# Kernel optimization log

Hardware: AMD Instinct MI355X
Metric: run time of the kernel (lower is better)

Reference implementation:

```python
import jax, jax.numpy as jnp
import numpy as np

V, E, H, L, B, T = 8192, 64, 256, 2, 4, 512


def setup_inputs() -> dict:
    key = jax.random.key(0)
    ks = jax.random.split(key, 20)
    s = 0.02
    emb = (jax.random.normal(ks[0], (V, E)) * s).at[0].set(0.0)  # padding_idx=0
    x = jax.random.randint(ks[1], (B, T), 0, V)
    return {
        "x": x,
        "emb": emb,
        "W_ih0": jax.random.normal(ks[2], (H, E)) * s,
        "W_hh0": jax.random.normal(ks[3], (H, H)) * s,
        "b_ih0": jnp.zeros((H,), jnp.float32),
        "b_hh0": jnp.zeros((H,), jnp.float32),
        "W_ih1": jax.random.normal(ks[4], (H, H)) * s,
        "W_hh1": jax.random.normal(ks[5], (H, H)) * s,
        "b_ih1": jnp.zeros((H,), jnp.float32),
        "b_hh1": jnp.zeros((H,), jnp.float32),
        "Wq": jax.random.normal(ks[6], (H, H)) * s,
        "Wk": jax.random.normal(ks[7], (H, H)) * s,
        "v": jax.random.normal(ks[8], (H,)) * s,
        "gamma": jnp.ones((2 * H,), jnp.float32),
        "beta": jnp.zeros((2 * H,), jnp.float32),
        "Wfc": jax.random.normal(ks[9], (V, 2 * H)) * s,
        "bfc": jnp.zeros((V,), jnp.float32),
    }


def _rnn_layer(xs, W_ih, W_hh, b_ih, b_hh):
    # xs: (B, T, D) -> ys: (B, T, H), hT: (B, H). Vanilla tanh RNN.
    Bn = xs.shape[0]
    Hn = W_hh.shape[0]
    h0 = jnp.zeros((Bn, Hn), xs.dtype)

    def step(h, xt):
        h_new = jnp.tanh(xt @ W_ih.T + b_ih + h @ W_hh.T + b_hh)
        return h_new, h_new

    hT, ys = jax.lax.scan(step, h0, jnp.swapaxes(xs, 0, 1))
    return jnp.swapaxes(ys, 0, 1), hT


def reference(x, emb, W_ih0, W_hh0, b_ih0, b_hh0, W_ih1, W_hh1, b_ih1, b_hh1,
              Wq, Wk, v, gamma, beta, Wfc, bfc):
    # Dropout layers are identity (eval mode).
    e = emb[x]                                   # (B, T, E)
    y0, h0 = _rnn_layer(e, W_ih0, W_hh0, b_ih0, b_hh0)
    y1, h1 = _rnn_layer(y0, W_ih1, W_hh1, b_ih1, b_hh1)  # (B, T, H)

    # Bahdanau additive attention with causal mask
    q = y1 @ Wq.T                                # (B, T, H)
    k = y1 @ Wk.T                                # (B, T, H)
    # (B, Tq, Tk, H) broadcast add -> tanh -> contract with v
    scores = jnp.einsum('bijh,h->bij', jnp.tanh(q[:, :, None, :] + k[:, None, :, :]), v)
    Tn = scores.shape[1]
    causal = jnp.tril(jnp.ones((Tn, Tn), bool))
    scores = jnp.where(causal[None], scores, jnp.float32(-1e9))
    alpha = jax.nn.softmax(scores, axis=-1)      # (B, Tq, Tk)
    ctx = jnp.einsum('bij,bjh->bih', alpha, y1)  # bmm(alpha, K) with K = rnn_out

    cat = jnp.concatenate([y1, ctx], axis=-1)    # (B, T, 2H)
    mu = cat.mean(-1, keepdims=True)
    var = ((cat - mu) ** 2).mean(-1, keepdims=True)
    normed = (cat - mu) / jnp.sqrt(var + 1e-5) * gamma + beta

    logits = normed @ Wfc.T + bfc                # (B, T, V)
    h = jnp.stack([h0, h1], axis=0)              # (L, B, H)
    return logits, h
```

## Files before the change

### kernel.cpp

```cpp
#include <hip/hip_runtime.h>
#include <hip/hip_bf16.h>

typedef __bf16 bf16x8 __attribute__((ext_vector_type(8)));
typedef float  f32x4  __attribute__((ext_vector_type(4)));
typedef unsigned short u16;

#define T_N 512
#define H_N 256
#define B_N 4
#define V_N 8192
#define E_N 64

__device__ __forceinline__ float tanh_fast(float x) {
    float e = __expf(2.0f * x);
    return 1.0f - __fdividef(2.0f, e + 1.0f);
}

__device__ __forceinline__ float tanh_pade(float x) {
    x = fminf(3.0f, fmaxf(-3.0f, x));
    float x2 = x * x;
    float num = x * (945.0f + x2 * (105.0f + x2));
    float den = 945.0f + x2 * (420.0f + 15.0f * x2);
    return num * __frcp_rn(den);
}

__device__ __forceinline__ u16 f2bf(float f) {
    __hip_bfloat16 h = __float2bfloat16(f);
    return __builtin_bit_cast(u16, h);
}

__device__ __forceinline__ bf16x8 as_bf16x8(uint4 u) {
    return __builtin_bit_cast(bf16x8, u);
}

__device__ __forceinline__ uint4 pack_bf8(f32x4 lo, f32x4 hi) {
    union { u16 s[8]; uint4 u; } r;
    #pragma unroll
    for (int e = 0; e < 4; ++e) { r.s[e] = f2bf(lo[e]); r.s[e+4] = f2bf(hi[e]); }
    return r.u;
}

__device__ __forceinline__ f32x4 mfma16(bf16x8 a, bf16x8 b, f32x4 c) {
    return __builtin_amdgcn_mfma_f32_16x16x32_bf16(a, b, c, 0, 0, 0);
}

__global__ void cvt_bf16_kernel(const float* __restrict__ src, u16* __restrict__ dst, int n4) {
    int i = blockIdx.x * 256 + threadIdx.x;
    if (i < n4) {
        f32x4 v = ((const f32x4*)src)[i];
        union { u16 s[4]; unsigned long long u; } r;
        #pragma unroll
        for (int e = 0; e < 4; ++e) r.s[e] = f2bf(v[e]);
        ((unsigned long long*)dst)[i] = r.u;
    }
}

__global__ __launch_bounds__(256)
void prep_wih1_kernel(const float* __restrict__ Wih1, uint4* __restrict__ out) {
    const int f = blockIdx.x * 256 + threadIdx.x;
    const int jt = f >> 9, kk = (f >> 6) & 7, lo = f & 63;
    const int mo = lo & 15, go = lo >> 4;
    const float* p = Wih1 + (size_t)(jt * 16 + mo) * H_N + (kk << 5) + (go << 3);
    f32x4 a = *(const f32x4*)p;
    f32x4 b = *(const f32x4*)(p + 4);
    out[f] = pack_bf8(a, b);
}

__global__ __launch_bounds__(256)
void embed_xw0_kernel(const int* __restrict__ x, const float* __restrict__ emb,
                      const float* __restrict__ Wih, const float* __restrict__ bih,
                      const float* __restrict__ bhh, float* __restrict__ xw0) {
    const int t = blockIdx.x, tid = threadIdx.x;
    __shared__ float sE[4][64];
    {
        const int b = tid >> 6, k = tid & 63;
        sE[b][k] = emb[(size_t)x[b * T_N + t] * E_N + k];
    }
    __syncthreads();
    const int j = tid;
    const float* wr = Wih + j * E_N;
    float a0 = 0, a1 = 0, a2 = 0, a3 = 0;
    #pragma unroll 8
    for (int k = 0; k < E_N; ++k) {
        float wv = wr[k];
        a0 += sE[0][k] * wv; a1 += sE[1][k] * wv;
        a2 += sE[2][k] * wv; a3 += sE[3][k] * wv;
    }
    const float bs = bih[j] + bhh[j];
    f32x4 o = { a0 + bs, a1 + bs, a2 + bs, a3 + bs };
    *(f32x4*)(xw0 + ((size_t)t * H_N + j) * 4) = o;
}

__global__ __launch_bounds__(512, 2)
void rnn_fused_kernel(const float* __restrict__ Whh0, const float* __restrict__ Whh1,
                      const uint4* __restrict__ xfg, const float* __restrict__ bih1,
                      const float* __restrict__ bhh1, const float* __restrict__ xw0,
                      u16* __restrict__ y1bf, float* __restrict__ y1f,
                      float* __restrict__ hT) {
    __shared__ __align__(16) u16   ring[8][4][288];
    __shared__ __align__(16) u16   h1b[2][4][288];
    __shared__ __align__(16) float xwb[2][4][256][4];

    const int tid = threadIdx.x;
    const int w = tid >> 6, l = tid & 63;
    const int m = l & 15, g = l >> 4, b4 = m & 3;
    const int layer = w >> 2, wl = w & 3;
    const int jmy = (wl << 6) + l;

    for (int i = tid; i < 8 * 4 * 288; i += 512) (&ring[0][0][0])[i] = (u16)0;
    for (int i = tid; i < 2 * 4 * 288; i += 512) (&h1b[0][0][0])[i] = (u16)0;

    const float* Whh = (layer == 0) ? Whh0 : Whh1;
    bf16x8 wfrag[4][8];
    #pragma unroll
    for (int nt = 0; nt < 4; ++nt) {
        const int j = (wl << 6) + (nt << 4) + m;
        #pragma unroll
        for (int kk = 0; kk < 8; ++kk) {
            const float* p = Whh + (size_t)j * H_N + (kk << 5) + (g << 3);
            f32x4 lo4 = *(const f32x4*)p;
            f32x4 hi4 = *(const f32x4*)(p + 4);
            wfrag[nt][kk] = as_bf16x8(pack_bf8(lo4, hi4));
        }
    }

    const float bias1 = bih1[jmy] + bhh1[jmy];
    const f32x4* xwv = (const f32x4*)xw0;
    f32x4 xw_cur = xwv[jmy];
    const uint4* xgw = xfg + ((size_t)w << 10);

    __syncthreads();

    for (int it = 0; it < 517; ++it) {
        const bool burst = ((it & 3) == 0) && (it >= 4) && (it <= 512);

        uint4 xf0[8];
        if (burst) {
            #pragma unroll
            for (int kk = 0; kk < 8; ++kk) xf0[kk] = xgw[(kk << 6) + l];
        }

        if (layer == 0) {
            if (it < 512) {
                const int tn = (it + 1 < 512) ? it + 1 : it;
                f32x4 xw_nxt = xwv[(size_t)tn * H_N + jmy];
                const int rs = (it - 1) & 7;

                bf16x8 af[8];
                #pragma unroll
                for (int kk = 0; kk < 8; ++kk)
                    af[kk] = as_bf16x8(*(const uint4*)&ring[rs][b4][(kk << 5) + (g << 3)]);

                f32x4 ca[4], cb[4];
                #pragma unroll
                for (int nt = 0; nt < 4; ++nt) {
                    ca[nt] = (f32x4){0.f, 0.f, 0.f, 0.f};
                    cb[nt] = (f32x4){0.f, 0.f, 0.f, 0.f};
                }
                #pragma unroll
                for (int kk = 0; kk < 4; ++kk)
                    #pragma unroll
                    for (int nt = 0; nt < 4; ++nt) {
                        ca[nt] = mfma16(af[kk],     wfrag[nt][kk],     ca[nt]);
                        cb[nt] = mfma16(af[kk + 4], wfrag[nt][kk + 4], cb[nt]);
                    }

                f32x4 hv = (g == 0) ? (ca[0] + cb[0])
                         : (g == 1) ? (ca[1] + cb[1])
                         : (g == 2) ? (ca[2] + cb[2])
                         :            (ca[3] + cb[3]);
                hv += xw_cur;

                #pragma unroll
                for (int b = 0; b < 4; ++b) {
                    float hn = tanh_fast(hv[b]);
                    ring[it & 7][b][jmy] = f2bf(hn);
                    if (it == T_N - 1) hT[b * H_N + jmy] = hn;
                }
                xw_cur = xw_nxt;
            }
        } else {
            if (it >= 5) {
                const int s = it - 5;
                f32x4 xws = *(const f32x4*)&xwb[(s >> 2) & 1][s & 3][jmy][0];
                const int rs = (s - 1) & 1;

                bf16x8 af[8];
                #pragma unroll
                for (int kk = 0; kk < 8; ++kk)
                    af[kk] = as_bf16x8(*(const uint4*)&h1b[rs][b4][(kk << 5) + (g << 3)]);

                f32x4 ca[4], cb[4];
                #pragma unroll
                for (int nt = 0; nt < 4; ++nt) {
                    ca[nt] = (f32x4){0.f, 0.f, 0.f, 0.f};
                    cb[nt] = (f32x4){0.f, 0.f, 0.f, 0.f};
                }
                #pragma unroll
                for (int kk = 0; kk < 4; ++kk)
                    #pragma unroll
                    for (int nt = 0; nt < 4; ++nt) {
                        ca[nt] = mfma16(af[kk],     wfrag[nt][kk],     ca[nt]);
                        cb[nt] = mfma16(af[kk + 4], wfrag[nt][kk + 4], cb[nt]);
                    }

                f32x4 hv = (g == 0) ? (ca[0] + cb[0])
                         : (g == 1) ? (ca[1] + cb[1])
                         : (g == 2) ? (ca[2] + cb[2])
                         :            (ca[3] + cb[3]);
                hv += xws;
                hv += (f32x4){bias1, bias1, bias1, bias1};

                #pragma unroll
                for (int b = 0; b < 4; ++b) {
                    float hn = tanh_fast(hv[b]);
                    u16 bits = f2bf(hn);
                    h1b[s & 1][b][jmy] = bits;
                    y1bf[((size_t)b * T_N + s) * H_N + jmy] = bits;
                    y1f [((size_t)b * T_N + s) * H_N + jmy] = hn;
                    if (s == T_N - 1) hT[1024 + b * H_N + jmy] = hn;
                }
            }
        }

        if (burst) {
            const int t0 = it - 4;
            const int par = ((it - 4) >> 2) & 1;
            const int slotm = (t0 + (m >> 2)) & 7;
            bf16x8 ax[8];
            #pragma unroll
            for (int kk = 0; kk < 8; ++kk)
                ax[kk] = as_bf16x8(*(const uint4*)&ring[slotm][b4][(kk << 5) + (g << 3)]);

            f32x4 xa0 = {0.f, 0.f, 0.f, 0.f};
            #pragma unroll
            for (int kk = 0; kk < 8; ++kk)
                xa0 = mfma16(ax[kk], as_bf16x8(xf0[kk]), xa0);

            uint4 xf1[8];
            #pragma unroll
            for (int kk = 0; kk < 8; ++kk) xf1[kk] = xgw[512 + (kk << 6) + l];

            f32x4 xa1 = {0.f, 0.f, 0.f, 0.f};
            #pragma unroll
            for (int kk = 0; kk < 8; ++kk)
                xa1 = mfma16(ax[kk], as_bf16x8(xf1[kk]), xa1);

            *(f32x4*)&xwb[par][g][(w << 5) + m][0]      = xa0;
            *(f32x4*)&xwb[par][g][(w << 5) + 16 + m][0] = xa1;
        }

        asm volatile("s_waitcnt lgkmcnt(0)\n\ts_barrier" ::: "memory");
    }
}

template<int MODE>
__global__ __launch_bounds__(256, 2)
void gemm_bf16(const u16* __restrict__ A, const u16* __restrict__ Bw,
               float* __restrict__ out, const float* __restrict__ bias,
               const float* __restrict__ bias2, int M, int N, int K) {
    __shared__ __align__(16) u16 As[64][40];
    __shared__ __align__(16) u16 Bs[64][40];
    const int tid = threadIdx.x;
    const int nb = N >> 6;
    const int bm = blockIdx.x / nb, bn = blockIdx.x % nb;
    const int l = tid & 63, w = tid >> 6;
    const int wm = w & 1, wn = w >> 1;
    const int m = l & 15, g = l >> 4;
    const int srow = tid >> 2, sseg = tid & 3;

    f32x4 c[2][2];
    #pragma unroll
    for (int i = 0; i < 2; ++i)
        #pragma unroll
        for (int j = 0; j < 2; ++j) c[i][j] = (f32x4){0.f, 0.f, 0.f, 0.f};

    const u16* ap = A  + (size_t)(bm * 64 + srow) * K + sseg * 8;
    const u16* bp = Bw + (size_t)(bn * 64 + srow) * K + sseg * 8;

    for (int k0 = 0; k0 < K; k0 += 32) {
        uint4 av = *(const uint4*)(ap + k0);
        uint4 bv = *(const uint4*)(bp + k0);
        __syncthreads();
        *(uint4*)&As[srow][sseg << 3] = av;
        *(uint4*)&Bs[srow][sseg << 3] = bv;
        __syncthreads();
        bf16x8 af[2], bfr[2];
        #pragma unroll
        for (int i = 0; i < 2; ++i) {
            af[i]  = as_bf16x8(*(const uint4*)&As[(wm << 5) + (i << 4) + m][g << 3]);
            bfr[i] = as_bf16x8(*(const uint4*)&Bs[(wn << 5) + (i << 4) + m][g << 3]);
        }
        #pragma unroll
        for (int i = 0; i < 2; ++i)
            #pragma unroll
            for (int j = 0; j < 2; ++j)
                c[i][j] = mfma16(af[i], bfr[j], c[i][j]);
    }

    #pragma unroll
    for (int i = 0; i < 2; ++i)
        #pragma unroll
        for (int j = 0; j < 2; ++j) {
            const int col = (bn << 6) + (wn << 5) + (j << 4) + m;
            float bs = 0.f;
            if (bias)  bs += bias[col];
            if (bias2) bs += bias2[col];
            #pragma unroll
            for (int r = 0; r < 4; ++r) {
                const int row = (bm << 6) + (wm << 5) + (i << 4) + (g << 2) + r;
                const float val = c[i][j][r] + bs;
                if (MODE == 0) {
                    out[(size_t)row * N + col] = val;
                } else {
                    const int b = row >> 9, t = row & 511;
                    out[(size_t)b * N * T_N + (size_t)col * T_N + t] = val;
                }
            }
        }
}

__global__ __launch_bounds__(256, 2)
void gemm_fc(const u16* __restrict__ A, const u16* __restrict__ Bw,
             const float* __restrict__ bias, float* __restrict__ out) {
    __shared__ __align__(16) u16 As[128 * 32];
    __shared__ __align__(16) u16 Bs[128 * 32];
    const int tid = threadIdx.x;
    const int l = tid & 63, w = tid >> 6;
    const int m = l & 15, g = l >> 4;
    const int wm = w >> 1, wn = w & 1;
    const int bm = blockIdx.x >> 6, bn = blockIdx.x & 63;
    constexpr int K = 512;

    f32x4 acc[4][4];
    #pragma unroll
    for (int i = 0; i < 4; ++i)
        #pragma unroll
        for (int j = 0; j < 4; ++j) acc[i][j] = (f32x4){0.f, 0.f, 0.f, 0.f};

    const u16* aBase = A  + (size_t)(bm * 128) * K;
    const u16* bBase = Bw + (size_t)(bn * 128) * K;
    const int row0 = tid >> 2,          seg0 = tid & 3;
    const int row1 = (tid + 256) >> 2,  seg1 = tid & 3;
    const int wseg0 = seg0 ^ ((row0 >> 1) & 3);
    const int wseg1 = seg1 ^ ((row1 >> 1) & 3);

    for (int k0 = 0; k0 < K; k0 += 32) {
        uint4 av0 = *(const uint4*)(aBase + (size_t)row0 * K + k0 + seg0 * 8);
        uint4 av1 = *(const uint4*)(aBase + (size_t)row1 * K + k0 + seg1 * 8);
        uint4 bv0 = *(const uint4*)(bBase + (size_t)row0 * K + k0 + seg0 * 8);
        uint4 bv1 = *(const uint4*)(bBase + (size_t)row1 * K + k0 + seg1 * 8);
        __syncthreads();
        *(uint4*)((char*)As + row0 * 64 + wseg0 * 16) = av0;
        *(uint4*)((char*)As + row1 * 64 + wseg1 * 16) = av1;
        *(uint4*)((char*)Bs + row0 * 64 + wseg0 * 16) = bv0;
        *(uint4*)((char*)Bs + row1 * 64 + wseg1 * 16) = bv1;
        __syncthreads();
        bf16x8 af[4], bfr[4];
        #pragma unroll
        for (int i = 0; i < 4; ++i) {
            const int arow = wm * 64 + i * 16 + m;
            const int aslot = g ^ ((arow >> 1) & 3);
            af[i]  = as_bf16x8(*(const uint4*)((char*)As + arow * 64 + aslot * 16));
            const int brow = wn * 64 + i * 16 + m;
            const int bslot = g ^ ((brow >> 1) & 3);
            bfr[i] = as_bf16x8(*(const uint4*)((char*)Bs + brow * 64 + bslot * 16));
        }
        #pragma unroll
        for (int i = 0; i < 4; ++i)
            #pragma unroll
            for (int j = 0; j < 4; ++j)
                acc[i][j] = mfma16(af[i], bfr[j], acc[i][j]);
    }

    #pragma unroll
    for (int i = 0; i < 4; ++i)
        #pragma unroll
        for (int j = 0; j < 4; ++j) {
            const int col = bn * 128 + wn * 64 + j * 16 + m;
            const float bs = bias[col];
            #pragma unroll
            for (int r = 0; r < 4; ++r) {
                const int row = bm * 128 + wm * 64 + i * 16 + (g << 2) + r;
                out[(size_t)row * V_N + col] = acc[i][j][r] + bs;
            }
        }
}

__global__ __launch_bounds__(256)
void attn_kernel(const float* __restrict__ q, const float* __restrict__ kT,
                 const float* __restrict__ y1f, const float* __restrict__ vvec,
                 float* __restrict__ ctx) {
    const int blk = blockIdx.x;
    const int b = blk >> 9, i = blk & 511;
    const int tid = threadIdx.x;
    __shared__ float sQ[H_N], sV[H_N], sS[T_N];
    __shared__ float red[4];
    sQ[tid] = q[((size_t)b * T_N + i) * H_N + tid];
    sV[tid] = vvec[tid];
    __syncthreads();

    float s0 = -1e30f, s1 = -1e30f;
    if (tid <= i) {
        const float* kp = kT + (size_t)b * H_N * T_N + tid;
        float acc = 0.f;
        for (int h = 0; h < H_N; ++h) acc += sV[h] * tanh_pade(sQ[h] + kp[(size_t)h * T_N]);
        s0 = acc;
    }
    if (tid + 256 <= i) {
        const float* kp = kT + (size_t)b * H_N * T_N + tid + 256;
        float acc = 0.f;
        for (int h = 0; h < H_N; ++h) acc += sV[h] * tanh_pade(sQ[h] + kp[(size_t)h * T_N]);
        s1 = acc;
    }
    float mv = fmaxf(s0, s1);
    #pragma unroll
    for (int o = 32; o; o >>= 1) mv = fmaxf(mv, __shfl_xor(mv, o, 64));
    if ((tid & 63) == 0) red[tid >> 6] = mv;
    __syncthreads();
    mv = fmaxf(fmaxf(red[0], red[1]), fmaxf(red[2], red[3]));
    __syncthreads();
    float e0 = (tid <= i)       ? __expf(s0 - mv) : 0.f;
    float e1 = (tid + 256 <= i) ? __expf(s1 - mv) : 0.f;
    float sm = e0 + e1;
    #pragma unroll
    for (int o = 32; o; o >>= 1) sm += __shfl_xor(sm, o, 64);
    if ((tid & 63) == 0) red[tid >> 6] = sm;
    __syncthreads();
    sm = red[0] + red[1] + red[2] + red[3];
    const float rs = 1.0f / sm;
    sS[tid] = e0 * rs;
    sS[tid + 256] = e1 * rs;
    __syncthreads();
    float acc = 0.f;
    const float* yp = y1f + (size_t)b * T_N * H_N + tid;
    for (int j2 = 0; j2 <= i; ++j2) acc += sS[j2] * yp[(size_t)j2 * H_N];
    ctx[((size_t)b * T_N + i) * H_N + tid] = acc;
}

__global__ __launch_bounds__(256)
void ln_kernel(const float* __restrict__ y1f, const float* __restrict__ ctx,
               const float* __restrict__ gamma, const float* __restrict__ beta,
               u16* __restrict__ outbf) {
    const int row = blockIdx.x, tid = threadIdx.x;
    __shared__ float red[4];
    const float x1 = y1f[(size_t)row * H_N + tid];
    const float x2 = ctx[(size_t)row * H_N + tid];
    float s = x1 + x2;
    #pragma unroll
    for (int o = 32; o; o >>= 1) s += __shfl_xor(s, o, 64);
    if ((tid & 63) == 0) red[tid >> 6] = s;
    __syncthreads();
    const float mu = (red[0] + red[1] + red[2] + red[3]) * (1.f / 512.f);
    __syncthreads();
    const float d1 = x1 - mu, d2 = x2 - mu;
    float qv = d1 * d1 + d2 * d2;
    #pragma unroll
    for (int o = 32; o; o >>= 1) qv += __shfl_xor(qv, o, 64);
    if ((tid & 63) == 0) red[tid >> 6] = qv;
    __syncthreads();
    const float var = (red[0] + red[1] + red[2] + red[3]) * (1.f / 512.f);
    const float inv = rsqrtf(var + 1e-5f);
    outbf[(size_t)row * 512 + tid]       = f2bf(d1 * inv * gamma[tid] + beta[tid]);
    outbf[(size_t)row * 512 + tid + 256] = f2bf(d2 * inv * gamma[tid + 256] + beta[tid + 256]);
}

extern "C" void kernel_launch(void* const* d_in, const int* in_sizes, int n_in,
                              void* d_out, int out_size, void* d_ws, size_t ws_size,
                              hipStream_t stream) {
    const int*   x     = (const int*)  d_in[0];
    const float* emb   = (const float*)d_in[1];
    const float* Wih0  = (const float*)d_in[2];
    const float* Whh0  = (const float*)d_in[3];
    const float* bih0  = (const float*)d_in[4];
    const float* bhh0  = (const float*)d_in[5];
    const float* Wih1  = (const float*)d_in[6];
    const float* Whh1  = (const float*)d_in[7];
    const float* bih1  = (const float*)d_in[8];
    const float* bhh1  = (const float*)d_in[9];
    const float* Wq    = (const float*)d_in[10];
    const float* Wk    = (const float*)d_in[11];
    const float* vvec  = (const float*)d_in[12];
    const float* gamma = (const float*)d_in[13];
    const float* beta  = (const float*)d_in[14];
    const float* Wfc   = (const float*)d_in[15];
    const float* bfc   = (const float*)d_in[16];

    float* outp = (float*)d_out;
    char* ws = (char*)d_ws;
    float* xw0   = (float*)(ws + 0);
    uint4* xfg   = (uint4*)(ws + 2097152);
    u16*   y1bf  = (u16*)  (ws + 5242880);
    float* y1f   = (float*)(ws + 6291456);
    float* qf    = (float*)(ws + 8388608);
    float* kT    = (float*)(ws + 10485760);
    float* ctx   = (float*)(ws + 12582912);
    u16*   nrm   = (u16*)  (ws + 14680064);
    u16*   Wqb   = (u16*)  (ws + 16908288);
    u16*   Wkb   = (u16*)  (ws + 17039360);
    u16*   Wfcb  = (u16*)  (ws + 17170432);

    float* hout = outp + (size_t)B_N * T_N * V_N;

    cvt_bf16_kernel<<<64,   256, 0, stream>>>(Wq,  Wqb,  65536 / 4);
    cvt_bf16_kernel<<<64,   256, 0, stream>>>(Wk,  Wkb,  65536 / 4);
    cvt_bf16_kernel<<<4096, 256, 0, stream>>>(Wfc, Wfcb, 4194304 / 4);
    prep_wih1_kernel<<<32, 256, 0, stream>>>(Wih1, xfg);

    embed_xw0_kernel<<<512, 256, 0, stream>>>(x, emb, Wih0, bih0, bhh0, xw0);
    rnn_fused_kernel<<<1, 512, 0, stream>>>(Whh0, Whh1, xfg, bih1, bhh1,
                                            xw0, y1bf, y1f, hout);
    gemm_bf16<0><<<32 * 4, 256, 0, stream>>>(y1bf, Wqb, qf, nullptr, nullptr, 2048, 256, 256);
    gemm_bf16<2><<<32 * 4, 256, 0, stream>>>(y1bf, Wkb, kT, nullptr, nullptr, 2048, 256, 256);
    attn_kernel<<<2048, 256, 0, stream>>>(qf, kT, y1f, vvec, ctx);
    ln_kernel<<<2048, 256, 0, stream>>>(y1f, ctx, gamma, beta, nrm);
    gemm_fc<<<16 * 64, 256, 0, stream>>>(nrm, Wfcb, bfc, outp);
}
```

Measured before the change: 854.7 us.

## Move layer-1 input projection bursts onto four dedicated wavefronts in RNN kernel

The fused two-layer RNN kernel grows from 512 to 768 threads. Four new wavefronts are dedicated to the periodic W_ih1 input-projection bursts, which the recurrent layer-0 and layer-1 wavefronts previously computed inline between their serial steps. The aim is to take the burst MFMA work and global weight loads off the critical recurrence path, so those waves only do the h@W_hh step each iteration. In exchange the block uses more threads and a lower register budget per thread under the new launch bounds, and it still synchronises all 12 waves with a barrier every step.

```diff
diff --git a/kernel.cpp b/kernel.cpp
--- a/kernel.cpp
+++ b/kernel.cpp
@@ -91,12 +91,12 @@
     *(f32x4*)(xw0 + ((size_t)t * H_N + j) * 4) = o;
 }
 
-__global__ __launch_bounds__(512, 2)
-void rnn_fused_kernel(const float* __restrict__ Whh0, const float* __restrict__ Whh1,
-                      const uint4* __restrict__ xfg, const float* __restrict__ bih1,
-                      const float* __restrict__ bhh1, const float* __restrict__ xw0,
-                      u16* __restrict__ y1bf, float* __restrict__ y1f,
-                      float* __restrict__ hT) {
+__global__ __launch_bounds__(768, 3)
+void rnn_fused12_kernel(const float* __restrict__ Whh0, const float* __restrict__ Whh1,
+                        const uint4* __restrict__ xfg, const float* __restrict__ bih1,
+                        const float* __restrict__ bhh1, const float* __restrict__ xw0,
+                        u16* __restrict__ y1bf, float* __restrict__ y1f,
+                        float* __restrict__ hT) {
     __shared__ __align__(16) u16   ring[8][4][288];
     __shared__ __align__(16) u16   h1b[2][4][288];
     __shared__ __align__(16) float xwb[2][4][256][4];
@@ -107,38 +107,34 @@
     const int layer = w >> 2, wl = w & 3;
     const int jmy = (wl << 6) + l;
 
-    for (int i = tid; i < 8 * 4 * 288; i += 512) (&ring[0][0][0])[i] = (u16)0;
-    for (int i = tid; i < 2 * 4 * 288; i += 512) (&h1b[0][0][0])[i] = (u16)0;
-
-    const float* Whh = (layer == 0) ? Whh0 : Whh1;
+    for (int i = tid; i < 8 * 4 * 288; i += 768) (&ring[0][0][0])[i] = (u16)0;
+    for (int i = tid; i < 2 * 4 * 288; i += 768) (&h1b[0][0][0])[i] = (u16)0;
+
     bf16x8 wfrag[4][8];
-    #pragma unroll
-    for (int nt = 0; nt < 4; ++nt) {
-        const int j = (wl << 6) + (nt << 4) + m;
-        #pragma unroll
-        for (int kk = 0; kk < 8; ++kk) {
-            const float* p = Whh + (size_t)j * H_N + (kk << 5) + (g << 3);
-            f32x4 lo4 = *(const f32x4*)p;
-            f32x4 hi4 = *(const f32x4*)(p + 4);
-            wfrag[nt][kk] = as_bf16x8(pack_bf8(lo4, hi4));
+    if (layer < 2) {
+        const float* Whh = (layer == 0) ? Whh0 : Whh1;
+        #pragma unroll
+        for (int nt = 0; nt < 4; ++nt) {
+            const int j = (wl << 6) + (nt << 4) + m;
+            #pragma unroll
+            for (int kk = 0; kk < 8; ++kk) {
+                const float* p = Whh + (size_t)j * H_N + (kk << 5) + (g << 3);
+                f32x4 lo4 = *(const f32x4*)p;
+                f32x4 hi4 = *(const f32x4*)(p + 4);
+                wfrag[nt][kk] = as_bf16x8(pack_bf8(lo4, hi4));
+            }
         }
     }
 
-    const float bias1 = bih1[jmy] + bhh1[jmy];
+    const float bias1 = bih1[jmy & 255] + bhh1[jmy & 255];
     const f32x4* xwv = (const f32x4*)xw0;
-    f32x4 xw_cur = xwv[jmy];
-    const uint4* xgw = xfg + ((size_t)w << 10);
+    f32x4 xw_cur = (layer == 0) ? xwv[jmy] : (f32x4){0.f, 0.f, 0.f, 0.f};
+    const int bw = w - 8;
 
     __syncthreads();
 
     for (int it = 0; it < 517; ++it) {
         const bool burst = ((it & 3) == 0) && (it >= 4) && (it <= 512);
-
-        uint4 xf0[8];
-        if (burst) {
-            #pragma unroll
-            for (int kk = 0; kk < 8; ++kk) xf0[kk] = xgw[(kk << 6) + l];
-        }
 
         if (layer == 0) {
             if (it < 512) {
@@ -179,7 +175,7 @@
                 }
                 xw_cur = xw_nxt;
             }
-        } else {
+        } else if (layer == 1) {
             if (it >= 5) {
                 const int s = it - 5;
                 f32x4 xws = *(const f32x4*)&xwb[(s >> 2) & 1][s & 3][jmy][0];
@@ -221,33 +217,39 @@
                     if (s == T_N - 1) hT[1024 + b * H_N + jmy] = hn;
                 }
             }
-        }
-
-        if (burst) {
-            const int t0 = it - 4;
-            const int par = ((it - 4) >> 2) & 1;
-            const int slotm = (t0 + (m >> 2)) & 7;
-            bf16x8 ax[8];
-            #pragma unroll
-            for (int kk = 0; kk < 8; ++kk)
-                ax[kk] = as_bf16x8(*(const uint4*)&ring[slotm][b4][(kk << 5) + (g << 3)]);
-
-            f32x4 xa0 = {0.f, 0.f, 0.f, 0.f};
-            #pragma unroll
-            for (int kk = 0; kk < 8; ++kk)
-                xa0 = mfma16(ax[kk], as_bf16x8(xf0[kk]), xa0);
-
-            uint4 xf1[8];
-            #pragma unroll
-            for (int kk = 0; kk < 8; ++kk) xf1[kk] = xgw[512 + (kk << 6) + l];
-
-            f32x4 xa1 = {0.f, 0.f, 0.f, 0.f};
-            #pragma unroll
-            for (int kk = 0; kk < 8; ++kk)
-                xa1 = mfma16(ax[kk], as_bf16x8(xf1[kk]), xa1);
-
-            *(f32x4*)&xwb[par][g][(w << 5) + m][0]      = xa0;
-            *(f32x4*)&xwb[par][g][(w << 5) + 16 + m][0] = xa1;
+        } else {
+            if (burst) {
+                const int t0 = it - 4;
+                const int par = (t0 >> 2) & 1;
+                const int slotm = (t0 + (m >> 2)) & 7;
+                bf16x8 ax[8];
+                #pragma unroll
+                for (int kk = 0; kk < 8; ++kk)
+                    ax[kk] = as_bf16x8(*(const uint4*)&ring[slotm][b4][(kk << 5) + (g << 3)]);
+
+                uint4 xfA[8], xfB[8];
+                #pragma unroll
+                for (int kk = 0; kk < 8; ++kk)
+                    xfA[kk] = xfg[(size_t)(((bw << 2) + 0) * 8 + kk) * 64 + l];
+                #pragma unroll
+                for (int t2 = 0; t2 < 4; ++t2) {
+                    if (t2 < 3) {
+                        #pragma unroll
+                        for (int kk = 0; kk < 8; ++kk)
+                            xfB[kk] = xfg[(size_t)(((bw << 2) + t2 + 1) * 8 + kk) * 64 + l];
+                    }
+                    f32x4 acc = {0.f, 0.f, 0.f, 0.f};
+                    #pragma unroll
+                    for (int kk = 0; kk < 8; ++kk)
+                        acc = mfma16(ax[kk], as_bf16x8(xfA[kk]), acc);
+                    const int col = (((bw << 2) + t2) << 4) + m;
+                    *(f32x4*)&xwb[par][g][col][0] = acc;
+                    if (t2 < 3) {
+                        #pragma unroll
+                        for (int kk = 0; kk < 8; ++kk) xfA[kk] = xfB[kk];
+                    }
+                }
+            }
         }
 
         asm volatile("s_waitcnt lgkmcnt(0)\n\ts_barrier" ::: "memory");
@@ -508,8 +510,8 @@
     prep_wih1_kernel<<<32, 256, 0, stream>>>(Wih1, xfg);
 
     embed_xw0_kernel<<<512, 256, 0, stream>>>(x, emb, Wih0, bih0, bhh0, xw0);
-    rnn_fused_kernel<<<1, 512, 0, stream>>>(Whh0, Whh1, xfg, bih1, bhh1,
-                                            xw0, y1bf, y1f, hout);
+    rnn_fused12_kernel<<<1, 768, 0, stream>>>(Whh0, Whh1, xfg, bih1, bhh1,
+                                              xw0, y1bf, y1f, hout);
     gemm_bf16<0><<<32 * 4, 256, 0, stream>>>(y1bf, Wqb, qf, nullptr, nullptr, 2048, 256, 256);
     gemm_bf16<2><<<32 * 4, 256, 0, stream>>>(y1bf, Wkb, kT, nullptr, nullptr, 2048, 256, 256);
     attn_kernel<<<2048, 256, 0, stream>>>(qf, kT, y1f, vvec, ctx);
```

After: 1.574 ms. 1.84x slower.
